# Kernel tuning notes

Measured on AMD Instinct MI355X. Metric: run time of the kernel, lower is better.

Reference implementation:

```python
import jax, jax.numpy as jnp
import numpy as np

BETA = 0.1       # reputation weight
GAMMA = 0.1      # load penalty weight
EXPL_C = 0.1     # UCB exploration constant
LOAD_EMA = 0.9   # load EMA alpha
TOP_K = 2
EPS = 1e-10


def setup_inputs() -> dict:
    key = jax.random.key(0)
    k1, k2, k3, k4, k5 = jax.random.split(key, 5)
    B, S, H, E = 4, 4096, 2048, 64
    return {
        "x": jax.random.normal(k1, (B, S, H), dtype=jnp.float32),
        "gate_w": jax.random.normal(k2, (E, H), dtype=jnp.float32) * (1.0 / np.sqrt(H)),
        "reputation": jax.random.normal(k3, (E,), dtype=jnp.float32),
        "loads": jax.random.uniform(k4, (E,), dtype=jnp.float32),
        "counts": jax.random.uniform(k5, (E,), dtype=jnp.float32),
        "total_decisions": 1000000,
    }


def reference(x, gate_w, reputation, loads, counts, total_decisions):
    B, S, H = x.shape
    E = gate_w.shape[0]
    x_flat = x.reshape(-1, H)                                  # [T, H]
    base_logits = jnp.einsum("th,eh->te", x_flat, gate_w)      # [T, E]

    # current_batch_assignments is None -> current_loads = expert_loads
    updated_loads = LOAD_EMA * loads + (1.0 - LOAD_EMA) * loads  # [E]

    # UCB-style exploration bonus, broadcast over tokens
    expl = EXPL_C * jnp.sqrt(jnp.log(jnp.float32(total_decisions) + 1.0) / (counts + EPS))  # [E]

    selection_scores = (base_logits
                        + BETA * reputation[None, :]
                        - GAMMA * updated_loads[None, :]
                        + expl[None, :])                        # [T, E]

    top_k_scores, top_k_indices = jax.lax.top_k(selection_scores, TOP_K)  # [T, K]
    routing_weights = jax.nn.softmax(top_k_scores, axis=-1).reshape(B, S, TOP_K)
    expert_indices = top_k_indices.reshape(B, S, TOP_K)

    # differentiable load-balancing aux loss
    router_probs = jax.nn.softmax(selection_scores.astype(jnp.float32), axis=-1)  # [T, E]
    expert_gate = jax.nn.one_hot(top_k_indices, E, dtype=jnp.float32).sum(axis=1)  # [T, E]
    tokens_per_expert = expert_gate.mean(axis=0)               # [E]
    router_prob_per_expert = router_probs.mean(axis=0)         # [E]
    aux_loss = (tokens_per_expert * router_prob_per_expert).sum() * E

    return routing_weights, expert_indices, aux_loss
```

## Files before the change

### kernel.cpp

```cpp
#include <hip/hip_runtime.h>
#include <cmath>

#define HDIM 2048
#define H4   (HDIM / 4)
#define NEXP 64
#define TTOT 16384
#define KSPLIT 2
#define KBLK (HDIM / KSPLIT)
#define BKC  64
#define NCHUNK (KBLK / BKC)
#define BTOK 64
#define LDT  72
#define LDS_SC 65

#define WS_PARTIAL_OFF 128
#define PARTIAL_FLOATS ((size_t)(TTOT / BTOK) * KSPLIT * BTOK * NEXP)

typedef short  bf16x8 __attribute__((ext_vector_type(8)));
typedef float  f32x4  __attribute__((ext_vector_type(4)));

__device__ __forceinline__ short f2bf_rn(float f, float* back) {
    unsigned u = __float_as_uint(f);
    unsigned r = (u + 0x7fffu + ((u >> 16) & 1u)) & 0xffff0000u;
    *back = __uint_as_float(r);
    return (short)(r >> 16);
}

__global__ __launch_bounds__(256, 2) void router_gemm_mfma(
    const float* __restrict__ x,
    const float* __restrict__ gw,
    float* __restrict__ partial)
{
    __shared__ short aT[3][BTOK][LDT];
    __shared__ short bT[3][NEXP][LDT];

    const int tid  = threadIdx.x;
    const int lane = tid & 63;
    const int quad = lane >> 4;
    const int l15  = lane & 15;
    const int w    = tid >> 6;
    const int wm   = w & 1;
    const int wn   = w >> 1;
    const int tb   = blockIdx.x;
    const int kg   = blockIdx.y;
    const int T0   = tb * BTOK;

    const int srow = tid >> 2;
    const int scol = tid & 3;

    const float4* __restrict__ x4 = reinterpret_cast<const float4*>(x);
    const float4* __restrict__ g4 = reinterpret_cast<const float4*>(gw);

    f32x4 acc[2][2];
    #pragma unroll
    for (int i = 0; i < 2; ++i)
        #pragma unroll
        for (int j = 0; j < 2; ++j)
            acc[i][j] = (f32x4){0.f, 0.f, 0.f, 0.f};

    float4 xa[4], xb[4];

#define LOAD_CHUNK(CH) do {                                                    \
        const int _c4b = kg * (H4 / 2) + (CH) * (BKC / 4);                     \
        _Pragma("unroll")                                                      \
        for (int j = 0; j < 4; ++j) {                                          \
            xa[j] = x4[(size_t)(T0 + srow) * H4 + _c4b + scol + 4 * j];        \
            xb[j] = g4[(size_t)srow * H4 + _c4b + scol + 4 * j];               \
        } } while (0)

#define SPLIT_STORE(TILE, ROW, KLOC, FV) do {                                  \
        const float _f[4] = {(FV).x, (FV).y, (FV).z, (FV).w};                  \
        short _h[4], _m[4], _l[4];                                             \
        _Pragma("unroll")                                                      \
        for (int u = 0; u < 4; ++u) {                                          \
            float _b0, _b1, _b2;                                               \
            _h[u] = f2bf_rn(_f[u], &_b0);                                      \
            float _r1 = _f[u] - _b0;                                           \
            _m[u] = f2bf_rn(_r1, &_b1);                                        \
            float _r2 = _r1 - _b1;                                             \
            _l[u] = f2bf_rn(_r2, &_b2);                                        \
        }                                                                      \
        *reinterpret_cast<short4*>(&TILE[0][ROW][KLOC]) =                      \
            make_short4(_h[0], _h[1], _h[2], _h[3]);                           \
        *reinterpret_cast<short4*>(&TILE[1][ROW][KLOC]) =                      \
            make_short4(_m[0], _m[1], _m[2], _m[3]);                           \
        *reinterpret_cast<short4*>(&TILE[2][ROW][KLOC]) =                      \
            make_short4(_l[0], _l[1], _l[2], _l[3]);                           \
    } while (0)

    LOAD_CHUNK(0);

    for (int ch = 0; ch < NCHUNK; ++ch) {
        #pragma unroll
        for (int j = 0; j < 4; ++j) {
            const int kloc = 4 * (scol + 4 * j);
            SPLIT_STORE(aT, srow, kloc, xa[j]);
            SPLIT_STORE(bT, srow, kloc, xb[j]);
        }
        __syncthreads();

        if (ch + 1 < NCHUNK) LOAD_CHUNK(ch + 1);

        #pragma unroll
        for (int k0 = 0; k0 < BKC; k0 += 32) {
            const int kf = k0 + quad * 8;
            bf16x8 ah[2], am[2], al[2], bh[2], bm[2], bl[2];
            #pragma unroll
            for (int mt = 0; mt < 2; ++mt) {
                const int row = 32 * wm + 16 * mt + l15;
                ah[mt] = *reinterpret_cast<const bf16x8*>(&aT[0][row][kf]);
                am[mt] = *reinterpret_cast<const bf16x8*>(&aT[1][row][kf]);
                al[mt] = *reinterpret_cast<const bf16x8*>(&aT[2][row][kf]);
            }
            #pragma unroll
            for (int nt = 0; nt < 2; ++nt) {
                const int row = 32 * wn + 16 * nt + l15;
                bh[nt] = *reinterpret_cast<const bf16x8*>(&bT[0][row][kf]);
                bm[nt] = *reinterpret_cast<const bf16x8*>(&bT[1][row][kf]);
                bl[nt] = *reinterpret_cast<const bf16x8*>(&bT[2][row][kf]);
            }
            #pragma unroll
            for (int mt = 0; mt < 2; ++mt)
                #pragma unroll
                for (int nt = 0; nt < 2; ++nt) {
                    f32x4 c = acc[mt][nt];
                    c = __builtin_amdgcn_mfma_f32_16x16x32_bf16(ah[mt], bh[nt], c, 0, 0, 0);
                    c = __builtin_amdgcn_mfma_f32_16x16x32_bf16(ah[mt], bm[nt], c, 0, 0, 0);
                    c = __builtin_amdgcn_mfma_f32_16x16x32_bf16(am[mt], bh[nt], c, 0, 0, 0);
                    c = __builtin_amdgcn_mfma_f32_16x16x32_bf16(ah[mt], bl[nt], c, 0, 0, 0);
                    c = __builtin_amdgcn_mfma_f32_16x16x32_bf16(am[mt], bm[nt], c, 0, 0, 0);
                    c = __builtin_amdgcn_mfma_f32_16x16x32_bf16(al[mt], bh[nt], c, 0, 0, 0);
                    acc[mt][nt] = c;
                }
        }
        __syncthreads();
    }
#undef LOAD_CHUNK
#undef SPLIT_STORE

    float* pbase = partial + ((size_t)tb * KSPLIT + kg) * (BTOK * NEXP);
    #pragma unroll
    for (int mt = 0; mt < 2; ++mt)
        #pragma unroll
        for (int nt = 0; nt < 2; ++nt) {
            const int e = 32 * wn + 16 * nt + l15;
            #pragma unroll
            for (int r = 0; r < 4; ++r) {
                const int t_loc = 32 * wm + 16 * mt + quad * 4 + r;
                pbase[(size_t)t_loc * NEXP + e] = acc[mt][nt][r];
            }
        }
}

__global__ __launch_bounds__(256) void router_reduce(
    const float* __restrict__ partial,
    const float* __restrict__ rep,
    const float* __restrict__ loads,
    const float* __restrict__ counts,
    const int*   __restrict__ total_dec,
    float* __restrict__ out_w,
    float* __restrict__ out_idx,
    float* __restrict__ prob_acc,
    float* __restrict__ gate_acc)
{
    __shared__ float sc_s[BTOK][LDS_SC];
    __shared__ float bias_s[NEXP];
    __shared__ float m_s[BTOK], z_s[BTOK];
    __shared__ int   i1_s[BTOK], i2_s[BTOK];

    const int tid = threadIdx.x;
    const int rt  = blockIdx.x;
    const int t0  = rt * BTOK;

    if (tid < NEXP) {
        float L = logf((float)(*total_dec) + 1.0f);
        bias_s[tid] = 0.1f * rep[tid] - 0.1f * loads[tid]
                    + 0.1f * sqrtf(L / (counts[tid] + 1e-10f));
    }
    __syncthreads();

    const float* p = partial + (size_t)rt * KSPLIT * (BTOK * NEXP);
    #pragma unroll
    for (int o = 0; o < (BTOK * NEXP) / 256; ++o) {
        const int idx = o * 256 + tid;
        float s = p[idx] + p[BTOK * NEXP + idx];
        sc_s[idx >> 6][idx & 63] = s + bias_s[idx & 63];
    }
    __syncthreads();

    if (tid < BTOK) {
        const int t = tid;
        float m1 = -INFINITY, m2 = -INFINITY;
        int   i1 = 0, i2 = 0;
        for (int e = 0; e < NEXP; ++e) {
            const float s = sc_s[t][e];
            if (s > m1)      { m2 = m1; i2 = i1; m1 = s; i1 = e; }
            else if (s > m2) { m2 = s; i2 = e; }
        }
        float z = 0.0f;
        for (int e = 0; e < NEXP; ++e) z += expf(sc_s[t][e] - m1);

        const float e2  = expf(m2 - m1);
        const float inv = 1.0f / (1.0f + e2);
        const int   gt  = t0 + t;
        reinterpret_cast<float2*>(out_w)[gt]   = make_float2(inv, e2 * inv);
        reinterpret_cast<float2*>(out_idx)[gt] = make_float2((float)i1, (float)i2);
        m_s[t] = m1; z_s[t] = z; i1_s[t] = i1; i2_s[t] = i2;
    }
    __syncthreads();

    if (tid < NEXP) {
        const int e = tid;
        float ps = 0.0f, gs = 0.0f;
        for (int t = 0; t < BTOK; ++t) {
            ps += expf(sc_s[t][e] - m_s[t]) / z_s[t];
            gs += (float)((i1_s[t] == e) + (i2_s[t] == e));
        }
        atomicAdd(&prob_acc[e], ps);
        atomicAdd(&gate_acc[e], gs);
    }
}

#define BKF  32
#define LDAF (64 + 4)
__global__ __launch_bounds__(256) void router_main(
    const float* __restrict__ x,
    const float* __restrict__ gw,
    const float* __restrict__ rep,
    const float* __restrict__ loads,
    const float* __restrict__ counts,
    const int*   __restrict__ total_dec,
    float* __restrict__ out_w,
    float* __restrict__ out_idx,
    float* __restrict__ prob_acc,
    float* __restrict__ gate_acc)
{
    __shared__ float a_s[2][BKF][LDAF];
    __shared__ float b_s[2][BKF][LDAF];
    __shared__ float sc_s[64][LDS_SC];
    __shared__ float bias_s[NEXP];
    __shared__ float m_s[64], z_s[64];
    __shared__ int   i1_s[64], i2_s[64];

    const int tid = threadIdx.x;
    const int tx  = tid & 15;
    const int ty  = tid >> 4;
    const int r0  = tid >> 3;
    const int c4  = tid & 7;
    const int t0  = blockIdx.x * 64;

    if (tid < NEXP) {
        float L = logf((float)(*total_dec) + 1.0f);
        bias_s[tid] = 0.1f * rep[tid] - 0.1f * loads[tid]
                    + 0.1f * sqrtf(L / (counts[tid] + 1e-10f));
    }

    const float4* __restrict__ x4 = reinterpret_cast<const float4*>(x) + (size_t)t0 * H4;
    const float4* __restrict__ g4 = reinterpret_cast<const float4*>(gw);

    float acc[4][4] = {};

#define STORE_TILE(BUFI, A0, A1, B0, B1) do {                                  \
        float _t0[4] = {(A0).x, (A0).y, (A0).z, (A0).w};                       \
        float _t1[4] = {(A1).x, (A1).y, (A1).z, (A1).w};                       \
        float _t2[4] = {(B0).x, (B0).y, (B0).z, (B0).w};                       \
        float _t3[4] = {(B1).x, (B1).y, (B1).z, (B1).w};                       \
        _Pragma("unroll")                                                      \
        for (int u = 0; u < 4; ++u) {                                          \
            a_s[BUFI][c4 * 4 + u][r0]      = _t0[u];                           \
            a_s[BUFI][c4 * 4 + u][r0 + 32] = _t1[u];                           \
            b_s[BUFI][c4 * 4 + u][r0]      = _t2[u];                           \
            b_s[BUFI][c4 * 4 + u][r0 + 32] = _t3[u];                           \
        } } while (0)

    {
        float4 a0 = x4[(size_t)r0 * H4 + c4];
        float4 a1 = x4[(size_t)(r0 + 32) * H4 + c4];
        float4 b0 = g4[(size_t)r0 * H4 + c4];
        float4 b1 = g4[(size_t)(r0 + 32) * H4 + c4];
        STORE_TILE(0, a0, a1, b0, b1);
    }
    __syncthreads();

    int buf = 0;
    for (int it = 0; it < HDIM / BKF; ++it) {
        float4 na0, na1, nb0, nb1;
        const bool has_next = (it + 1 < HDIM / BKF);
        if (has_next) {
            const int k4 = (it + 1) * (BKF / 4);
            na0 = x4[(size_t)r0 * H4 + k4 + c4];
            na1 = x4[(size_t)(r0 + 32) * H4 + k4 + c4];
            nb0 = g4[(size_t)r0 * H4 + k4 + c4];
            nb1 = g4[(size_t)(r0 + 32) * H4 + k4 + c4];
        }
        #pragma unroll
        for (int kk = 0; kk < BKF; ++kk) {
            const float4 afv = *reinterpret_cast<const float4*>(&a_s[buf][kk][ty * 4]);
            const float4 bfv = *reinterpret_cast<const float4*>(&b_s[buf][kk][tx * 4]);
            const float af[4] = {afv.x, afv.y, afv.z, afv.w};
            const float bf[4] = {bfv.x, bfv.y, bfv.z, bfv.w};
            #pragma unroll
            for (int i = 0; i < 4; ++i)
                #pragma unroll
                for (int j = 0; j < 4; ++j)
                    acc[i][j] = fmaf(af[i], bf[j], acc[i][j]);
        }
        if (has_next) STORE_TILE(buf ^ 1, na0, na1, nb0, nb1);
        __syncthreads();
        buf ^= 1;
    }
#undef STORE_TILE

    #pragma unroll
    for (int i = 0; i < 4; ++i)
        #pragma unroll
        for (int j = 0; j < 4; ++j)
            sc_s[ty * 4 + i][tx * 4 + j] = acc[i][j] + bias_s[tx * 4 + j];
    __syncthreads();

    if (tid < 64) {
        const int t = tid;
        float m1 = -INFINITY, m2 = -INFINITY;
        int   i1 = 0, i2 = 0;
        for (int e = 0; e < NEXP; ++e) {
            const float s = sc_s[t][e];
            if (s > m1)      { m2 = m1; i2 = i1; m1 = s; i1 = e; }
            else if (s > m2) { m2 = s; i2 = e; }
        }
        float z = 0.0f;
        for (int e = 0; e < NEXP; ++e) z += expf(sc_s[t][e] - m1);
        const float e2  = expf(m2 - m1);
        const float inv = 1.0f / (1.0f + e2);
        const int   gt  = t0 + t;
        reinterpret_cast<float2*>(out_w)[gt]   = make_float2(inv, e2 * inv);
        reinterpret_cast<float2*>(out_idx)[gt] = make_float2((float)i1, (float)i2);
        m_s[t] = m1; z_s[t] = z; i1_s[t] = i1; i2_s[t] = i2;
    }
    __syncthreads();

    if (tid < NEXP) {
        const int e = tid;
        float ps = 0.0f, gs = 0.0f;
        for (int t = 0; t < 64; ++t) {
            ps += expf(sc_s[t][e] - m_s[t]) / z_s[t];
            gs += (float)((i1_s[t] == e) + (i2_s[t] == e));
        }
        atomicAdd(&prob_acc[e], ps);
        atomicAdd(&gate_acc[e], gs);
    }
}

__global__ void router_aux(const float* __restrict__ prob_acc,
                           const float* __restrict__ gate_acc,
                           float* __restrict__ out_aux)
{
    const float invT = 1.0f / (float)TTOT;
    const int e = threadIdx.x;
    float v = (gate_acc[e] * invT) * (prob_acc[e] * invT);
    #pragma unroll
    for (int off = 32; off > 0; off >>= 1)
        v += __shfl_down(v, off);
    if (e == 0) out_aux[0] = v * (float)NEXP;
}

extern "C" void kernel_launch(void* const* d_in, const int* in_sizes, int n_in,
                              void* d_out, int out_size, void* d_ws, size_t ws_size,
                              hipStream_t stream)
{
    const float* x      = (const float*)d_in[0];
    const float* gw     = (const float*)d_in[1];
    const float* rep    = (const float*)d_in[2];
    const float* loads  = (const float*)d_in[3];
    const float* counts = (const float*)d_in[4];
    const int*   total  = (const int*)d_in[5];

    float* out     = (float*)d_out;
    float* out_w   = out;
    float* out_idx = out + 32768;
    float* out_aux = out + 65536;

    float* prob_acc = (float*)d_ws;
    float* gate_acc = prob_acc + NEXP;
    float* partial  = (float*)d_ws + WS_PARTIAL_OFF;

    const size_t ws_needed = (WS_PARTIAL_OFF + PARTIAL_FLOATS) * sizeof(float);

    hipMemsetAsync(d_ws, 0, WS_PARTIAL_OFF * sizeof(float), stream);

    if (ws_size >= ws_needed) {
        router_gemm_mfma<<<dim3(TTOT / BTOK, KSPLIT), dim3(256), 0, stream>>>(x, gw, partial);
        router_reduce<<<dim3(TTOT / BTOK), dim3(256), 0, stream>>>(
            partial, rep, loads, counts, total, out_w, out_idx, prob_acc, gate_acc);
    } else {
        router_main<<<dim3(TTOT / 64), dim3(256), 0, stream>>>(
            x, gw, rep, loads, counts, total, out_w, out_idx, prob_acc, gate_acc);
    }
    router_aux<<<dim3(1), dim3(64), 0, stream>>>(prob_acc, gate_acc, out_aux);
}
```

Measured before the change: 232.9 us.

## Pre-split gate weights once and load MFMA fragments directly from global memory

Result: slower. 278.7 us (+19.7%).

```diff
diff --git a/kernel.cpp b/kernel.cpp
--- a/kernel.cpp
+++ b/kernel.cpp
@@ -7,33 +7,66 @@
 #define TTOT 16384
 #define KSPLIT 2
 #define KBLK (HDIM / KSPLIT)
-#define BKC  64
-#define NCHUNK (KBLK / BKC)
+#define NSTEP (KBLK / 32)
 #define BTOK 64
-#define LDT  72
 #define LDS_SC 65
 
 #define WS_PARTIAL_OFF 128
 #define PARTIAL_FLOATS ((size_t)(TTOT / BTOK) * KSPLIT * BTOK * NEXP)
+#define GWSZ (NEXP * HDIM)
 
 typedef short  bf16x8 __attribute__((ext_vector_type(8)));
 typedef float  f32x4  __attribute__((ext_vector_type(4)));
-
-__device__ __forceinline__ short f2bf_rn(float f, float* back) {
-    unsigned u = __float_as_uint(f);
-    unsigned r = (u + 0x7fffu + ((u >> 16) & 1u)) & 0xffff0000u;
-    *back = __uint_as_float(r);
-    return (short)(r >> 16);
+typedef int    i32x4  __attribute__((ext_vector_type(4)));
+
+__device__ __forceinline__ void split8(const float4 f0, const float4 f1,
+                                       bf16x8* h, bf16x8* m, bf16x8* l)
+{
+    const float f[8] = {f0.x, f0.y, f0.z, f0.w, f1.x, f1.y, f1.z, f1.w};
+    unsigned uh[8], um[8], ul[8];
+    #pragma unroll
+    for (int i = 0; i < 8; ++i) {
+        const unsigned u = __float_as_uint(f[i]);
+        uh[i] = u & 0xffff0000u;
+        const float r1 = f[i] - __uint_as_float(uh[i]);
+        um[i] = __float_as_uint(r1) & 0xffff0000u;
+        const float r2 = r1 - __uint_as_float(um[i]);
+        ul[i] = __float_as_uint(r2) & 0xffff0000u;
+    }
+    i32x4 vh, vm, vl;
+    #pragma unroll
+    for (int j = 0; j < 4; ++j) {
+        vh[j] = (int)((uh[2*j] >> 16) | uh[2*j+1]);
+        vm[j] = (int)((um[2*j] >> 16) | um[2*j+1]);
+        vl[j] = (int)((ul[2*j] >> 16) | ul[2*j+1]);
+    }
+    *h = *reinterpret_cast<bf16x8*>(&vh);
+    *m = *reinterpret_cast<bf16x8*>(&vm);
+    *l = *reinterpret_cast<bf16x8*>(&vl);
+}
+
+__global__ __launch_bounds__(256) void split_gw_kernel(
+    const float* __restrict__ gw,
+    short* __restrict__ gwh, short* __restrict__ gwm, short* __restrict__ gwl)
+{
+    const int g   = blockIdx.x * 256 + threadIdx.x;
+    const int idx = g * 8;
+    const float4 f0 = *reinterpret_cast<const float4*>(gw + idx);
+    const float4 f1 = *reinterpret_cast<const float4*>(gw + idx + 4);
+    bf16x8 h, m, l;
+    split8(f0, f1, &h, &m, &l);
+    *reinterpret_cast<bf16x8*>(gwh + idx) = h;
+    *reinterpret_cast<bf16x8*>(gwm + idx) = m;
+    *reinterpret_cast<bf16x8*>(gwl + idx) = l;
 }
 
 __global__ __launch_bounds__(256, 2) void router_gemm_mfma(
     const float* __restrict__ x,
-    const float* __restrict__ gw,
+    const short* __restrict__ gwh,
+    const short* __restrict__ gwm,
+    const short* __restrict__ gwl,
     float* __restrict__ partial)
 {
-    __shared__ short aT[3][BTOK][LDT];
-    __shared__ short bT[3][NEXP][LDT];
-
     const int tid  = threadIdx.x;
     const int lane = tid & 63;
     const int quad = lane >> 4;
@@ -45,11 +78,18 @@
     const int kg   = blockIdx.y;
     const int T0   = tb * BTOK;
 
-    const int srow = tid >> 2;
-    const int scol = tid & 3;
-
     const float4* __restrict__ x4 = reinterpret_cast<const float4*>(x);
-    const float4* __restrict__ g4 = reinterpret_cast<const float4*>(gw);
+
+    size_t arow[2];
+    #pragma unroll
+    for (int mt = 0; mt < 2; ++mt)
+        arow[mt] = (size_t)(T0 + 32 * wm + 16 * mt + l15) * H4
+                 + (size_t)kg * (H4 / 2) + quad * 2;
+
+    int brow[2];
+    #pragma unroll
+    for (int nt = 0; nt < 2; ++nt)
+        brow[nt] = (32 * wn + 16 * nt + l15) * HDIM + kg * KBLK + quad * 8;
 
     f32x4 acc[2][2];
     #pragma unroll
@@ -58,85 +98,37 @@
         for (int j = 0; j < 2; ++j)
             acc[i][j] = (f32x4){0.f, 0.f, 0.f, 0.f};
 
-    float4 xa[4], xb[4];
-
-#define LOAD_CHUNK(CH) do {                                                    \
-        const int _c4b = kg * (H4 / 2) + (CH) * (BKC / 4);                     \
-        _Pragma("unroll")                                                      \
-        for (int j = 0; j < 4; ++j) {                                          \
-            xa[j] = x4[(size_t)(T0 + srow) * H4 + _c4b + scol + 4 * j];        \
-            xb[j] = g4[(size_t)srow * H4 + _c4b + scol + 4 * j];               \
-        } } while (0)
-
-#define SPLIT_STORE(TILE, ROW, KLOC, FV) do {                                  \
-        const float _f[4] = {(FV).x, (FV).y, (FV).z, (FV).w};                  \
-        short _h[4], _m[4], _l[4];                                             \
-        _Pragma("unroll")                                                      \
-        for (int u = 0; u < 4; ++u) {                                          \
-            float _b0, _b1, _b2;                                               \
-            _h[u] = f2bf_rn(_f[u], &_b0);                                      \
-            float _r1 = _f[u] - _b0;                                           \
-            _m[u] = f2bf_rn(_r1, &_b1);                                        \
-            float _r2 = _r1 - _b1;                                             \
-            _l[u] = f2bf_rn(_r2, &_b2);                                        \
-        }                                                                      \
-        *reinterpret_cast<short4*>(&TILE[0][ROW][KLOC]) =                      \
-            make_short4(_h[0], _h[1], _h[2], _h[3]);                           \
-        *reinterpret_cast<short4*>(&TILE[1][ROW][KLOC]) =                      \
-            make_short4(_m[0], _m[1], _m[2], _m[3]);                           \
-        *reinterpret_cast<short4*>(&TILE[2][ROW][KLOC]) =                      \
-            make_short4(_l[0], _l[1], _l[2], _l[3]);                           \
-    } while (0)
-
-    LOAD_CHUNK(0);
-
-    for (int ch = 0; ch < NCHUNK; ++ch) {
-        #pragma unroll
-        for (int j = 0; j < 4; ++j) {
-            const int kloc = 4 * (scol + 4 * j);
-            SPLIT_STORE(aT, srow, kloc, xa[j]);
-            SPLIT_STORE(bT, srow, kloc, xb[j]);
-        }
-        __syncthreads();
-
-        if (ch + 1 < NCHUNK) LOAD_CHUNK(ch + 1);
-
-        #pragma unroll
-        for (int k0 = 0; k0 < BKC; k0 += 32) {
-            const int kf = k0 + quad * 8;
-            bf16x8 ah[2], am[2], al[2], bh[2], bm[2], bl[2];
-            #pragma unroll
-            for (int mt = 0; mt < 2; ++mt) {
-                const int row = 32 * wm + 16 * mt + l15;
-                ah[mt] = *reinterpret_cast<const bf16x8*>(&aT[0][row][kf]);
-                am[mt] = *reinterpret_cast<const bf16x8*>(&aT[1][row][kf]);
-                al[mt] = *reinterpret_cast<const bf16x8*>(&aT[2][row][kf]);
-            }
+    #pragma unroll 2
+    for (int s = 0; s < NSTEP; ++s) {
+        bf16x8 bh[2], bm[2], bl[2];
+        #pragma unroll
+        for (int nt = 0; nt < 2; ++nt) {
+            const int o = brow[nt] + s * 32;
+            bh[nt] = *reinterpret_cast<const bf16x8*>(gwh + o);
+            bm[nt] = *reinterpret_cast<const bf16x8*>(gwm + o);
+            bl[nt] = *reinterpret_cast<const bf16x8*>(gwl + o);
+        }
+        bf16x8 ah[2], am[2], al[2];
+        #pragma unroll
+        for (int mt = 0; mt < 2; ++mt) {
+            const float4 f0 = x4[arow[mt] + (size_t)s * 8];
+            const float4 f1 = x4[arow[mt] + (size_t)s * 8 + 1];
+            split8(f0, f1, &ah[mt], &am[mt], &al[mt]);
+        }
+        #pragma unroll
+        for (int mt = 0; mt < 2; ++mt)
             #pragma unroll
             for (int nt = 0; nt < 2; ++nt) {
-                const int row = 32 * wn + 16 * nt + l15;
-                bh[nt] = *reinterpret_cast<const bf16x8*>(&bT[0][row][kf]);
-                bm[nt] = *reinterpret_cast<const bf16x8*>(&bT[1][row][kf]);
-                bl[nt] = *reinterpret_cast<const bf16x8*>(&bT[2][row][kf]);
+                f32x4 c = acc[mt][nt];
+                c = __builtin_amdgcn_mfma_f32_16x16x32_bf16(ah[mt], bh[nt], c, 0, 0, 0);
+                c = __builtin_amdgcn_mfma_f32_16x16x32_bf16(ah[mt], bm[nt], c, 0, 0, 0);
+                c = __builtin_amdgcn_mfma_f32_16x16x32_bf16(am[mt], bh[nt], c, 0, 0, 0);
+                c = __builtin_amdgcn_mfma_f32_16x16x32_bf16(ah[mt], bl[nt], c, 0, 0, 0);
+                c = __builtin_amdgcn_mfma_f32_16x16x32_bf16(am[mt], bm[nt], c, 0, 0, 0);
+                c = __builtin_amdgcn_mfma_f32_16x16x32_bf16(al[mt], bh[nt], c, 0, 0, 0);
+                acc[mt][nt] = c;
             }
-            #pragma unroll
-            for (int mt = 0; mt < 2; ++mt)
-                #pragma unroll
-                for (int nt = 0; nt < 2; ++nt) {
-                    f32x4 c = acc[mt][nt];
-                    c = __builtin_amdgcn_mfma_f32_16x16x32_bf16(ah[mt], bh[nt], c, 0, 0, 0);
-                    c = __builtin_amdgcn_mfma_f32_16x16x32_bf16(ah[mt], bm[nt], c, 0, 0, 0);
-                    c = __builtin_amdgcn_mfma_f32_16x16x32_bf16(am[mt], bh[nt], c, 0, 0, 0);
-                    c = __builtin_amdgcn_mfma_f32_16x16x32_bf16(ah[mt], bl[nt], c, 0, 0, 0);
-                    c = __builtin_amdgcn_mfma_f32_16x16x32_bf16(am[mt], bm[nt], c, 0, 0, 0);
-                    c = __builtin_amdgcn_mfma_f32_16x16x32_bf16(al[mt], bh[nt], c, 0, 0, 0);
-                    acc[mt][nt] = c;
-                }
-        }
-        __syncthreads();
-    }
-#undef LOAD_CHUNK
-#undef SPLIT_STORE
+    }
 
     float* pbase = partial + ((size_t)tb * KSPLIT + kg) * (BTOK * NEXP);
     #pragma unroll
@@ -382,13 +374,20 @@
     float* prob_acc = (float*)d_ws;
     float* gate_acc = prob_acc + NEXP;
     float* partial  = (float*)d_ws + WS_PARTIAL_OFF;
-
-    const size_t ws_needed = (WS_PARTIAL_OFF + PARTIAL_FLOATS) * sizeof(float);
+    short* gwsplit  = (short*)((float*)d_ws + WS_PARTIAL_OFF + PARTIAL_FLOATS);
+    short* gwh = gwsplit;
+    short* gwm = gwsplit + GWSZ;
+    short* gwl = gwsplit + 2 * GWSZ;
+
+    const size_t ws_needed = (WS_PARTIAL_OFF + PARTIAL_FLOATS) * sizeof(float)
+                           + 3 * GWSZ * sizeof(short);
 
     hipMemsetAsync(d_ws, 0, WS_PARTIAL_OFF * sizeof(float), stream);
 
     if (ws_size >= ws_needed) {
-        router_gemm_mfma<<<dim3(TTOT / BTOK, KSPLIT), dim3(256), 0, stream>>>(x, gw, partial);
+        split_gw_kernel<<<dim3(GWSZ / (256 * 8)), dim3(256), 0, stream>>>(gw, gwh, gwm, gwl);
+        router_gemm_mfma<<<dim3(TTOT / BTOK, KSPLIT), dim3(256), 0, stream>>>(
+            x, gwh, gwm, gwl, partial);
         router_reduce<<<dim3(TTOT / BTOK), dim3(256), 0, stream>>>(
             partial, rep, loads, counts, total, out_w, out_idx, prob_acc, gate_acc);
     } else {
```
